# Performance work log

Measured on AMD Instinct MI355X. Metric: run time of the kernel, lower is better.

Reference implementation:

```python
import jax, jax.numpy as jnp
import numpy as np

B, T, N, C = 4, 16, 256, 768
H = 12
D = C // H
HID = 4 * C
SCALE = D ** -0.5
EPS = 1e-5


def _layernorm(x, g, b):
    mu = jnp.mean(x, axis=-1, keepdims=True)
    var = jnp.var(x, axis=-1, keepdims=True)
    return (x - mu) * jax.lax.rsqrt(var + EPS) * g + b


def setup_inputs() -> dict:
    key = jax.random.key(0)
    ks = jax.random.split(key, 12)
    s = 0.02
    return {
        "x": jax.random.normal(ks[0], (B, T, N, C), dtype=jnp.float32),
        "ln1s_g": jnp.ones((C,), jnp.float32), "ln1s_b": jnp.zeros((C,), jnp.float32),
        "ln1t_g": jnp.ones((C,), jnp.float32), "ln1t_b": jnp.zeros((C,), jnp.float32),
        "ln2_g": jnp.ones((C,), jnp.float32), "ln2_b": jnp.zeros((C,), jnp.float32),
        "Wqkv_s": jax.random.normal(ks[1], (C, 3 * C), jnp.float32) * s,
        "Wproj_s": jax.random.normal(ks[2], (C, C), jnp.float32) * s,
        "bproj_s": jnp.zeros((C,), jnp.float32),
        "Wqkv_t": jax.random.normal(ks[3], (C, 3 * C), jnp.float32) * s,
        "Wproj_t": jax.random.normal(ks[4], (C, C), jnp.float32) * s,
        "bproj_t": jnp.zeros((C,), jnp.float32),
        "Wfc1": jax.random.normal(ks[5], (C, HID), jnp.float32) * s,
        "bfc1": jnp.zeros((HID,), jnp.float32),
        "Wfc2": jax.random.normal(ks[6], (HID, C), jnp.float32) * s,
        "bfc2": jnp.zeros((C,), jnp.float32),
    }


def _spatial_attn(x, Wqkv, Wproj, bproj):
    b, t, n, c = x.shape
    qkv = (x @ Wqkv).reshape(b, t, n, 3, H, D)
    q, k, v = jnp.moveaxis(qkv, 3, 0)  # each (B,T,N,H,D)
    attn = jnp.einsum('btnhd,btmhd->bthnm', q, k) * SCALE
    a = jax.nn.softmax(attn, axis=-1)
    o = jnp.einsum('bthnm,btmhd->btnhd', a, v).reshape(b, t, n, c)
    return o @ Wproj + bproj


def _temporal_attn(x, Wqkv, Wproj, bproj):
    b, t, n, c = x.shape
    qkv = (x @ Wqkv).reshape(b, t, n, 3, H, D)
    q, k, v = jnp.moveaxis(qkv, 3, 0)  # each (B,T,N,H,D)
    attn = jnp.einsum('btnhd,bsnhd->bnhts', q, k) * SCALE
    causal = jnp.triu(jnp.ones((t, t), dtype=bool), k=1)  # (T,T) upper mask
    attn = jnp.where(causal, -jnp.inf, attn)
    a = jax.nn.softmax(attn, axis=-1)
    o = jnp.einsum('bnhts,bsnhd->btnhd', a, v).reshape(b, t, n, c)
    return o @ Wproj + bproj


def _mlp(x, W1, b1, W2, b2):
    h = jax.nn.gelu(x @ W1 + b1, approximate=False)
    return h @ W2 + b2


def reference(x, ln1s_g, ln1s_b, ln1t_g, ln1t_b, ln2_g, ln2_b,
              Wqkv_s, Wproj_s, bproj_s, Wqkv_t, Wproj_t, bproj_t,
              Wfc1, bfc1, Wfc2, bfc2):
    x = x + _spatial_attn(_layernorm(x, ln1s_g, ln1s_b), Wqkv_s, Wproj_s, bproj_s)
    x = x + _temporal_attn(_layernorm(x, ln1t_g, ln1t_b), Wqkv_t, Wproj_t, bproj_t)
    x = x + _mlp(_layernorm(x, ln2_g, ln2_b), Wfc1, bfc1, Wfc2, bfc2)
    return x
```

## Files before the change

kernel.cpp:

```cpp
#include <hip/hip_runtime.h>

typedef unsigned short u16;
typedef __attribute__((ext_vector_type(8))) __bf16 bf16x8;
typedef __attribute__((ext_vector_type(4))) float f32x4;
typedef __attribute__((ext_vector_type(4))) u16 u16x4;

#define DEVI static __device__ __forceinline__

DEVI u16 f2bf(float f) {
    unsigned u = __float_as_uint(f);
    u += 0x7fffu + ((u >> 16) & 1u);
    return (u16)(u >> 16);
}
DEVI float bf2f(u16 b) { return __uint_as_float(((unsigned)b) << 16); }

DEVI void gll16(const void* g, void* s) {
    __builtin_amdgcn_global_load_lds((__attribute__((address_space(1))) void*)(g),
                                     (__attribute__((address_space(3))) void*)(s),
                                     16, 0, 0);
}

__global__ __launch_bounds__(256) void wtrans(const float* __restrict__ in,
                                              u16* __restrict__ out, int K, int N) {
    __shared__ float tile[32][33];
    int t = threadIdx.x;
    int n0 = blockIdx.x * 32, k0 = blockIdx.y * 32;
    int r = t >> 3, c4 = (t & 7) << 2;
    float4 v = *(const float4*)(in + (size_t)(k0 + r) * N + n0 + c4);
    tile[r][c4 + 0] = v.x; tile[r][c4 + 1] = v.y;
    tile[r][c4 + 2] = v.z; tile[r][c4 + 3] = v.w;
    __syncthreads();
    u16x4 o;
    o.x = f2bf(tile[c4 + 0][r]);
    o.y = f2bf(tile[c4 + 1][r]);
    o.z = f2bf(tile[c4 + 2][r]);
    o.w = f2bf(tile[c4 + 3][r]);
    *(u16x4*)(out + (size_t)(n0 + r) * K + k0 + c4) = o;
}

__global__ __launch_bounds__(256) void ln_bf16(const float* __restrict__ x,
                                               const float* __restrict__ g,
                                               const float* __restrict__ b,
                                               u16* __restrict__ out) {
    int l = threadIdx.x & 63;
    size_t row = (size_t)blockIdx.x * 4 + (threadIdx.x >> 6);
    const float4* xr = (const float4*)(x + row * 768);
    float4 vv[3];
    vv[0] = xr[l]; vv[1] = xr[l + 64]; vv[2] = xr[l + 128];
    float s = 0.f, ss = 0.f;
#pragma unroll
    for (int i = 0; i < 3; ++i) {
        s  += vv[i].x + vv[i].y + vv[i].z + vv[i].w;
        ss += vv[i].x * vv[i].x + vv[i].y * vv[i].y + vv[i].z * vv[i].z + vv[i].w * vv[i].w;
    }
#pragma unroll
    for (int m = 1; m < 64; m <<= 1) { s += __shfl_xor(s, m); ss += __shfl_xor(ss, m); }
    float mean = s * (1.f / 768.f);
    float rstd = rsqrtf(ss * (1.f / 768.f) - mean * mean + 1e-5f);
    const float4* gr = (const float4*)g;
    const float4* br = (const float4*)b;
    u16* orow = out + row * 768;
#pragma unroll
    for (int i = 0; i < 3; ++i) {
        float4 gv = gr[l + i * 64], bv = br[l + i * 64];
        u16x4 o;
        o.x = f2bf((vv[i].x - mean) * rstd * gv.x + bv.x);
        o.y = f2bf((vv[i].y - mean) * rstd * gv.y + bv.y);
        o.z = f2bf((vv[i].z - mean) * rstd * gv.z + bv.z);
        o.w = f2bf((vv[i].w - mean) * rstd * gv.w + bv.w);
        *(u16x4*)(orow + l * 4 + i * 256) = o;
    }
}

template <int HAS_BIAS, int HAS_RES, int DO_GELU, int OUT_BF16>
__global__ __launch_bounds__(256, 2) void gemm_bf16(const u16* __restrict__ A,
                                                    const u16* __restrict__ BT,
                                                    const float* __restrict__ bias,
                                                    const float* res,
                                                    void* outp, int M, int N, int K) {
    __shared__ __attribute__((aligned(16))) u16 lds_a[128 * 64];
    __shared__ __attribute__((aligned(16))) u16 lds_b[128 * 64];
    const int tid = threadIdx.x, l = tid & 63, w = tid >> 6;
    const int wr = w >> 1, wc = w & 1;
    const int lr = l & 15, lk8 = (l >> 4) * 8;
    const int m0 = blockIdx.y * 128, n0 = blockIdx.x * 128;
    const f32x4 FZ = {0.f, 0.f, 0.f, 0.f};
    f32x4 acc[4][4];
#pragma unroll
    for (int mi = 0; mi < 4; ++mi)
#pragma unroll
        for (int ni = 0; ni < 4; ++ni) acc[mi][ni] = FZ;

    const int nkt = K >> 6;
    for (int kt = 0; kt < nkt; ++kt) {
#pragma unroll
        for (int it = 0; it < 4; ++it) {
            int ci = it * 256 + tid;
            int rowa = ci >> 3, sl = ci & 7;
            gll16(A  + (size_t)(m0 + rowa) * K + kt * 64 + sl * 8, lds_a + ci * 8);
            gll16(BT + (size_t)(n0 + rowa) * K + kt * 64 + sl * 8, lds_b + ci * 8);
        }
        __syncthreads();
#pragma unroll
        for (int ks = 0; ks < 2; ++ks) {
            bf16x8 av[4], bv[4];
#pragma unroll
            for (int mi = 0; mi < 4; ++mi)
                av[mi] = *(const bf16x8*)&lds_a[(wr * 64 + mi * 16 + lr) * 64 + ks * 32 + lk8];
#pragma unroll
            for (int ni = 0; ni < 4; ++ni)
                bv[ni] = *(const bf16x8*)&lds_b[(wc * 64 + ni * 16 + lr) * 64 + ks * 32 + lk8];
#pragma unroll
            for (int mi = 0; mi < 4; ++mi)
#pragma unroll
                for (int ni = 0; ni < 4; ++ni)
                    acc[mi][ni] = __builtin_amdgcn_mfma_f32_16x16x32_bf16(av[mi], bv[ni],
                                                                          acc[mi][ni], 0, 0, 0);
        }
        __syncthreads();
    }
#pragma unroll
    for (int mi = 0; mi < 4; ++mi)
#pragma unroll
        for (int ni = 0; ni < 4; ++ni) {
            int col = n0 + wc * 64 + ni * 16 + lr;
            float bs = HAS_BIAS ? bias[col] : 0.f;
#pragma unroll
            for (int r = 0; r < 4; ++r) {
                int row = m0 + wr * 64 + mi * 16 + (l >> 4) * 4 + r;
                float v = acc[mi][ni][r] + bs;
                if (DO_GELU) v = 0.5f * v * (1.f + erff(v * 0.70710678118654752f));
                size_t idx = (size_t)row * N + col;
                if (HAS_RES) v += res[idx];
                if (OUT_BF16) ((u16*)outp)[idx] = f2bf(v);
                else          ((float*)outp)[idx] = v;
            }
        }
}

__global__ __launch_bounds__(256, 2) void sattn(const u16* __restrict__ qkv,
                                                u16* __restrict__ attno) {
    __shared__ __attribute__((aligned(16))) u16 p_lds[4][16][264];
    __shared__ __attribute__((aligned(16))) u16 vt_lds[64][264];
    const int tid = threadIdx.x, l = tid & 63, w = tid >> 6;
    const int lr = l & 15, lg = l >> 4;
    const int bid = blockIdx.x;
    const int h = bid % 12;
    const size_t R0 = (size_t)(bid / 12) * 256;
    const u16* base = qkv + R0 * 2304;
    const f32x4 FZ = {0.f, 0.f, 0.f, 0.f};

    {
        const u16* vrow = base + (size_t)tid * 2304 + 1536 + h * 64;
#pragma unroll
        for (int c = 0; c < 8; ++c) {
            bf16x8 vv = *(const bf16x8*)(vrow + c * 8);
            const u16* pv = (const u16*)&vv;
#pragma unroll
            for (int e = 0; e < 8; ++e) vt_lds[c * 8 + e][tid] = pv[e];
        }
    }
    __syncthreads();

    u16* attbase = attno + R0 * 768 + h * 64;
    for (int qb = 0; qb < 4; ++qb) {
        const int qrow0 = qb * 64 + w * 16;
        f32x4 acc[16];
#pragma unroll
        for (int nt = 0; nt < 16; ++nt) acc[nt] = FZ;
        const u16* qp = base + (size_t)(qrow0 + lr) * 2304 + h * 64;
#pragma unroll
        for (int ks = 0; ks < 2; ++ks) {
            bf16x8 af = *(const bf16x8*)(qp + ks * 32 + lg * 8);
#pragma unroll
            for (int nt = 0; nt < 16; ++nt) {
                const u16* kp = base + (size_t)(nt * 16 + lr) * 2304 + 768 + h * 64 + ks * 32 + lg * 8;
                bf16x8 bfr = *(const bf16x8*)kp;
                acc[nt] = __builtin_amdgcn_mfma_f32_16x16x32_bf16(af, bfr, acc[nt], 0, 0, 0);
            }
        }
#pragma unroll
        for (int r = 0; r < 4; ++r) {
            float m = acc[0][r] * 0.125f;
#pragma unroll
            for (int nt = 0; nt < 16; ++nt) { acc[nt][r] *= 0.125f; m = fmaxf(m, acc[nt][r]); }
            m = fmaxf(m, __shfl_xor(m, 1));
            m = fmaxf(m, __shfl_xor(m, 2));
            m = fmaxf(m, __shfl_xor(m, 4));
            m = fmaxf(m, __shfl_xor(m, 8));
            float ssum = 0.f;
#pragma unroll
            for (int nt = 0; nt < 16; ++nt) {
                float e = __expf(acc[nt][r] - m);
                acc[nt][r] = e; ssum += e;
            }
            ssum += __shfl_xor(ssum, 1);
            ssum += __shfl_xor(ssum, 2);
            ssum += __shfl_xor(ssum, 4);
            ssum += __shfl_xor(ssum, 8);
            float inv = 1.f / ssum;
#pragma unroll
            for (int nt = 0; nt < 16; ++nt) acc[nt][r] *= inv;
        }
#pragma unroll
        for (int nt = 0; nt < 16; ++nt)
#pragma unroll
            for (int r = 0; r < 4; ++r)
                p_lds[w][lg * 4 + r][nt * 16 + lr] = f2bf(acc[nt][r]);
        __syncthreads();
        f32x4 oacc[4];
#pragma unroll
        for (int dt = 0; dt < 4; ++dt) oacc[dt] = FZ;
#pragma unroll
        for (int ks = 0; ks < 8; ++ks) {
            bf16x8 af = *(const bf16x8*)&p_lds[w][lr][ks * 32 + lg * 8];
#pragma unroll
            for (int dt = 0; dt < 4; ++dt) {
                bf16x8 bfr = *(const bf16x8*)&vt_lds[dt * 16 + lr][ks * 32 + lg * 8];
                oacc[dt] = __builtin_amdgcn_mfma_f32_16x16x32_bf16(af, bfr, oacc[dt], 0, 0, 0);
            }
        }
#pragma unroll
        for (int dt = 0; dt < 4; ++dt)
#pragma unroll
            for (int r = 0; r < 4; ++r)
                attbase[(size_t)(qrow0 + lg * 4 + r) * 768 + dt * 16 + lr] = f2bf(oacc[dt][r]);
        __syncthreads();
    }
}

__global__ __launch_bounds__(256, 4) void tattn(const u16* __restrict__ qkv,
                                                u16* __restrict__ attno) {
    __shared__ float p_lds[4][16][17];
    const int tid = threadIdx.x, l = tid & 63, wv = tid >> 6;
    const int gw = blockIdx.x * 4 + wv;
    const int h = gw % 12;
    const int bn = gw / 12;
    const int n = bn & 255, b = bn >> 8;
    const u16* base = qkv + ((size_t)(b * 16) * 256 + n) * 2304;
    const size_t tstr = (size_t)256 * 2304;
    const int tk = l & 15, g = l >> 4;

    bf16x8 kv[8];
    const u16* kp = base + (size_t)tk * tstr + 768 + h * 64;
#pragma unroll
    for (int c = 0; c < 8; ++c) kv[c] = *(const bf16x8*)(kp + c * 8);

#pragma unroll
    for (int pass = 0; pass < 4; ++pass) {
        int tq = pass * 4 + g;
        const u16* qp = base + (size_t)tq * tstr + h * 64;
        float s = 0.f;
#pragma unroll
        for (int c = 0; c < 8; ++c) {
            bf16x8 qv = *(const bf16x8*)(qp + c * 8);
#pragma unroll
            for (int e = 0; e < 8; ++e) s += (float)qv[e] * (float)kv[c][e];
        }
        s = (tk <= tq) ? s * 0.125f : -1e30f;
        float m = s;
        m = fmaxf(m, __shfl_xor(m, 1));
        m = fmaxf(m, __shfl_xor(m, 2));
        m = fmaxf(m, __shfl_xor(m, 4));
        m = fmaxf(m, __shfl_xor(m, 8));
        float p = __expf(s - m);
        float ssum = p;
        ssum += __shfl_xor(ssum, 1);
        ssum += __shfl_xor(ssum, 2);
        ssum += __shfl_xor(ssum, 4);
        ssum += __shfl_xor(ssum, 8);
        p_lds[wv][tq][tk] = p / ssum;
    }
    __syncthreads();
    float vreg[16];
#pragma unroll
    for (int t2 = 0; t2 < 16; ++t2)
        vreg[t2] = bf2f(base[(size_t)t2 * tstr + 1536 + h * 64 + l]);
    u16* ob = attno + ((size_t)(b * 16) * 256 + n) * 768 + h * 64 + l;
#pragma unroll
    for (int tq = 0; tq < 16; ++tq) {
        float o = 0.f;
#pragma unroll
        for (int t2 = 0; t2 < 16; ++t2) o += p_lds[wv][tq][t2] * vreg[t2];
        ob[(size_t)tq * 256 * 768] = f2bf(o);
    }
}

extern "C" void kernel_launch(void* const* d_in, const int* in_sizes, int n_in,
                              void* d_out, int out_size, void* d_ws, size_t ws_size,
                              hipStream_t stream) {
    (void)in_sizes; (void)n_in; (void)out_size; (void)ws_size;
    const float* x       = (const float*)d_in[0];
    const float* ln1s_g  = (const float*)d_in[1];
    const float* ln1s_b  = (const float*)d_in[2];
    const float* ln1t_g  = (const float*)d_in[3];
    const float* ln1t_b  = (const float*)d_in[4];
    const float* ln2_g   = (const float*)d_in[5];
    const float* ln2_b   = (const float*)d_in[6];
    const float* Wqkv_s  = (const float*)d_in[7];
    const float* Wproj_s = (const float*)d_in[8];
    const float* bproj_s = (const float*)d_in[9];
    const float* Wqkv_t  = (const float*)d_in[10];
    const float* Wproj_t = (const float*)d_in[11];
    const float* bproj_t = (const float*)d_in[12];
    const float* Wfc1    = (const float*)d_in[13];
    const float* bfc1    = (const float*)d_in[14];
    const float* Wfc2    = (const float*)d_in[15];
    const float* bfc2    = (const float*)d_in[16];
    float* out = (float*)d_out;

    const int M = 16384, C = 768, HID = 3072, NQKV = 2304;

    char* p = (char*)d_ws;
    auto carve = [&](size_t bytes) {
        char* r = p;
        p += (bytes + 255) & ~(size_t)255;
        return r;
    };
    u16* wqkvT_s  = (u16*)carve((size_t)NQKV * C * 2);
    u16* wprojT_s = (u16*)carve((size_t)C * C * 2);
    u16* wqkvT_t  = (u16*)carve((size_t)NQKV * C * 2);
    u16* wprojT_t = (u16*)carve((size_t)C * C * 2);
    u16* wfc1T    = (u16*)carve((size_t)HID * C * 2);
    u16* wfc2T    = (u16*)carve((size_t)C * HID * 2);
    u16* xn       = (u16*)carve((size_t)M * C * 2);
    u16* attno    = (u16*)carve((size_t)M * C * 2);
    u16* big      = (u16*)carve((size_t)M * HID * 2);

    wtrans<<<dim3(NQKV / 32, C / 32), 256, 0, stream>>>(Wqkv_s, wqkvT_s, C, NQKV);
    wtrans<<<dim3(C / 32, C / 32), 256, 0, stream>>>(Wproj_s, wprojT_s, C, C);
    wtrans<<<dim3(NQKV / 32, C / 32), 256, 0, stream>>>(Wqkv_t, wqkvT_t, C, NQKV);
    wtrans<<<dim3(C / 32, C / 32), 256, 0, stream>>>(Wproj_t, wprojT_t, C, C);
    wtrans<<<dim3(HID / 32, C / 32), 256, 0, stream>>>(Wfc1, wfc1T, C, HID);
    wtrans<<<dim3(C / 32, HID / 32), 256, 0, stream>>>(Wfc2, wfc2T, HID, C);

    ln_bf16<<<M / 4, 256, 0, stream>>>(x, ln1s_g, ln1s_b, xn);
    gemm_bf16<0, 0, 0, 1><<<dim3(NQKV / 128, M / 128), 256, 0, stream>>>(
        xn, wqkvT_s, nullptr, nullptr, big, M, NQKV, C);
    sattn<<<768, 256, 0, stream>>>(big, attno);
    gemm_bf16<1, 1, 0, 0><<<dim3(C / 128, M / 128), 256, 0, stream>>>(
        attno, wprojT_s, bproj_s, x, out, M, C, C);

    ln_bf16<<<M / 4, 256, 0, stream>>>(out, ln1t_g, ln1t_b, xn);
    gemm_bf16<0, 0, 0, 1><<<dim3(NQKV / 128, M / 128), 256, 0, stream>>>(
        xn, wqkvT_t, nullptr, nullptr, big, M, NQKV, C);
    tattn<<<12288 / 4, 256, 0, stream>>>(big, attno);
    gemm_bf16<1, 1, 0, 0><<<dim3(C / 128, M / 128), 256, 0, stream>>>(
        attno, wprojT_t, bproj_t, out, out, M, C, C);

    ln_bf16<<<M / 4, 256, 0, stream>>>(out, ln2_g, ln2_b, xn);
    gemm_bf16<1, 0, 1, 1><<<dim3(HID / 128, M / 128), 256, 0, stream>>>(
        xn, wfc1T, bfc1, nullptr, big, M, HID, C);
    gemm_bf16<1, 1, 0, 0><<<dim3(C / 128, M / 128), 256, 0, stream>>>(
        big, wfc2T, bfc2, out, out, M, C, HID);
}
```

Before: 648.1 us.

## Replace 128x128 GEMM with pipelined 256x256 double-buffered MFMA kernel

Every dense GEMM now uses a new 512-thread kernel that computes 256x256 output tiles. It double-buffers LDS tiles filled by global_load_lds, issuing loads for later K steps while MFMAs run on the current buffer. The kernel also raises wave priority around MFMA bursts and remaps block IDs across XCDs to improve L2 locality. In exchange, the larger tiles give far fewer blocks for the C=768-wide GEMMs (192 on a 256-CU part), and 128KB of LDS limits occupancy to about one block per CU.

Result: slower. 719.8 us (+11.1%).

```diff
diff --git a/kernel.cpp b/kernel.cpp
--- a/kernel.cpp
+++ b/kernel.cpp
@@ -72,63 +72,130 @@
     }
 }
 
+#define MFMA_(a, b, c) __builtin_amdgcn_mfma_f32_16x16x32_bf16(a, b, c, 0, 0, 0)
+#define BAR() do { __builtin_amdgcn_sched_barrier(0); __builtin_amdgcn_s_barrier(); \
+                   __builtin_amdgcn_sched_barrier(0); } while (0)
+
 template <int HAS_BIAS, int HAS_RES, int DO_GELU, int OUT_BF16>
-__global__ __launch_bounds__(256, 2) void gemm_bf16(const u16* __restrict__ A,
-                                                    const u16* __restrict__ BT,
-                                                    const float* __restrict__ bias,
-                                                    const float* res,
-                                                    void* outp, int M, int N, int K) {
-    __shared__ __attribute__((aligned(16))) u16 lds_a[128 * 64];
-    __shared__ __attribute__((aligned(16))) u16 lds_b[128 * 64];
-    const int tid = threadIdx.x, l = tid & 63, w = tid >> 6;
-    const int wr = w >> 1, wc = w & 1;
-    const int lr = l & 15, lk8 = (l >> 4) * 8;
-    const int m0 = blockIdx.y * 128, n0 = blockIdx.x * 128;
+__global__ __launch_bounds__(512, 2) void gemm256(const u16* __restrict__ A,
+                                                  const u16* __restrict__ BT,
+                                                  const float* __restrict__ bias,
+                                                  const float* res, void* outp,
+                                                  int M, int N, int K, int nbx) {
+    __shared__ __attribute__((aligned(16))) u16 lds_s[2][2][2][8192];
+    const int tid = threadIdx.x, l = tid & 63, wid = tid >> 6;
+    const int l15 = l & 15, lhi = l >> 4;
+    const int wr = wid >> 2, wcn = wid & 3;
+    const int nwg = gridDim.x, orig = blockIdx.x;
+    const int qq = nwg >> 3, xcd = orig & 7, ii = orig >> 3;
+    const int swz = xcd * qq + ii;
+    const int bx = swz % nbx, by = swz / nbx;
+    const int m0 = by * 256, n0 = bx * 256;
+    const int nkt = K >> 6;
+
+    const u16* pA0 = A + (size_t)(m0 + wid * 32 + l15) * K + lhi * 8;
+    const u16* pA1 = pA0 + (size_t)16 * K;
+    const u16* pB0 = BT + (size_t)(n0 + wid * 32 + l15) * K + lhi * 8;
+    const u16* pB1 = pB0 + (size_t)16 * K;
+
+#define STAGE(D, MAT, KS, KT) do {                                          \
+        const int _ko = (KT) * 64 + (KS) * 32;                              \
+        u16* _dst = &lds_s[D][MAT][KS][wid * 1024];                         \
+        gll16(((MAT) ? pB0 : pA0) + _ko, _dst);                             \
+        gll16(((MAT) ? pB1 : pA1) + _ko, _dst + 512);                       \
+    } while (0)
+
+#define LDA_(D, KS, MF) (*(const bf16x8*)&lds_s[D][0][KS][(wr * 8 + (MF)) * 512 + l * 8])
+#define LDB_(D, KS, NF) (*(const bf16x8*)&lds_s[D][1][KS][(wcn * 4 + (NF)) * 512 + l * 8])
+#define LDA4(D, KS, MLO) do { av[0] = LDA_(D, KS, (MLO) + 0); av[1] = LDA_(D, KS, (MLO) + 1); \
+                              av[2] = LDA_(D, KS, (MLO) + 2); av[3] = LDA_(D, KS, (MLO) + 3); } while (0)
+#define LDB4(D, KS) do { bv[0] = LDB_(D, KS, 0); bv[1] = LDB_(D, KS, 1);    \
+                         bv[2] = LDB_(D, KS, 2); bv[3] = LDB_(D, KS, 3); } while (0)
+#define MM16(MLO) do {                                                      \
+        __builtin_amdgcn_s_setprio(1);                                      \
+        acc[(MLO)+0][0] = MFMA_(av[0], bv[0], acc[(MLO)+0][0]);             \
+        acc[(MLO)+0][1] = MFMA_(av[0], bv[1], acc[(MLO)+0][1]);             \
+        acc[(MLO)+0][2] = MFMA_(av[0], bv[2], acc[(MLO)+0][2]);             \
+        acc[(MLO)+0][3] = MFMA_(av[0], bv[3], acc[(MLO)+0][3]);             \
+        acc[(MLO)+1][0] = MFMA_(av[1], bv[0], acc[(MLO)+1][0]);             \
+        acc[(MLO)+1][1] = MFMA_(av[1], bv[1], acc[(MLO)+1][1]);             \
+        acc[(MLO)+1][2] = MFMA_(av[1], bv[2], acc[(MLO)+1][2]);             \
+        acc[(MLO)+1][3] = MFMA_(av[1], bv[3], acc[(MLO)+1][3]);             \
+        acc[(MLO)+2][0] = MFMA_(av[2], bv[0], acc[(MLO)+2][0]);             \
+        acc[(MLO)+2][1] = MFMA_(av[2], bv[1], acc[(MLO)+2][1]);             \
+        acc[(MLO)+2][2] = MFMA_(av[2], bv[2], acc[(MLO)+2][2]);             \
+        acc[(MLO)+2][3] = MFMA_(av[2], bv[3], acc[(MLO)+2][3]);             \
+        acc[(MLO)+3][0] = MFMA_(av[3], bv[0], acc[(MLO)+3][0]);             \
+        acc[(MLO)+3][1] = MFMA_(av[3], bv[1], acc[(MLO)+3][1]);             \
+        acc[(MLO)+3][2] = MFMA_(av[3], bv[2], acc[(MLO)+3][2]);             \
+        acc[(MLO)+3][3] = MFMA_(av[3], bv[3], acc[(MLO)+3][3]);             \
+        __builtin_amdgcn_s_setprio(0);                                      \
+    } while (0)
+
+    f32x4 acc[8][4];
     const f32x4 FZ = {0.f, 0.f, 0.f, 0.f};
-    f32x4 acc[4][4];
-#pragma unroll
-    for (int mi = 0; mi < 4; ++mi)
-#pragma unroll
-        for (int ni = 0; ni < 4; ++ni) acc[mi][ni] = FZ;
-
-    const int nkt = K >> 6;
-    for (int kt = 0; kt < nkt; ++kt) {
-#pragma unroll
-        for (int it = 0; it < 4; ++it) {
-            int ci = it * 256 + tid;
-            int rowa = ci >> 3, sl = ci & 7;
-            gll16(A  + (size_t)(m0 + rowa) * K + kt * 64 + sl * 8, lds_a + ci * 8);
-            gll16(BT + (size_t)(n0 + rowa) * K + kt * 64 + sl * 8, lds_b + ci * 8);
-        }
-        __syncthreads();
-#pragma unroll
-        for (int ks = 0; ks < 2; ++ks) {
-            bf16x8 av[4], bv[4];
-#pragma unroll
-            for (int mi = 0; mi < 4; ++mi)
-                av[mi] = *(const bf16x8*)&lds_a[(wr * 64 + mi * 16 + lr) * 64 + ks * 32 + lk8];
-#pragma unroll
-            for (int ni = 0; ni < 4; ++ni)
-                bv[ni] = *(const bf16x8*)&lds_b[(wc * 64 + ni * 16 + lr) * 64 + ks * 32 + lk8];
-#pragma unroll
-            for (int mi = 0; mi < 4; ++mi)
-#pragma unroll
-                for (int ni = 0; ni < 4; ++ni)
-                    acc[mi][ni] = __builtin_amdgcn_mfma_f32_16x16x32_bf16(av[mi], bv[ni],
-                                                                          acc[mi][ni], 0, 0, 0);
-        }
-        __syncthreads();
-    }
-#pragma unroll
-    for (int mi = 0; mi < 4; ++mi)
-#pragma unroll
-        for (int ni = 0; ni < 4; ++ni) {
-            int col = n0 + wc * 64 + ni * 16 + lr;
-            float bs = HAS_BIAS ? bias[col] : 0.f;
+#pragma unroll
+    for (int mf = 0; mf < 8; ++mf)
+#pragma unroll
+        for (int nf = 0; nf < 4; ++nf) acc[mf][nf] = FZ;
+
+    STAGE(0, 1, 0, 0);
+    STAGE(0, 0, 0, 0);
+    STAGE(0, 1, 1, 0);
+    STAGE(0, 0, 1, 0);
+    STAGE(1, 1, 0, 1);
+    STAGE(1, 0, 0, 1);
+    STAGE(1, 1, 1, 1);
+    asm volatile("s_waitcnt vmcnt(6)" ::: "memory");
+    BAR();
+
+    const int nit = nkt >> 1;
+    for (int it = 0; it < nit; ++it) {
+        const int kt0 = it * 2;
+        const int kt2 = (kt0 + 2 < nkt) ? kt0 + 2 : nkt - 1;
+        const int kt3 = (kt0 + 3 < nkt) ? kt0 + 3 : nkt - 1;
+        bf16x8 av[4], bv[4];
+        LDB4(0, 0); LDA4(0, 0, 0);
+        STAGE(1, 0, 1, kt0 + 1);
+        BAR(); MM16(0); BAR();
+        LDA4(0, 0, 4);
+        STAGE(0, 1, 0, kt2);
+        BAR(); MM16(4); BAR();
+        LDB4(0, 1); LDA4(0, 1, 0);
+        STAGE(0, 0, 0, kt2);
+        BAR(); MM16(0); BAR();
+        LDA4(0, 1, 4);
+        STAGE(0, 1, 1, kt2);
+        BAR(); MM16(4);
+        asm volatile("s_waitcnt vmcnt(6)" ::: "memory");
+        BAR();
+        LDB4(1, 0); LDA4(1, 0, 0);
+        STAGE(0, 0, 1, kt2);
+        BAR(); MM16(0); BAR();
+        LDA4(1, 0, 4);
+        STAGE(1, 1, 0, kt3);
+        BAR(); MM16(4); BAR();
+        LDB4(1, 1); LDA4(1, 1, 0);
+        STAGE(1, 0, 0, kt3);
+        BAR(); MM16(0); BAR();
+        LDA4(1, 1, 4);
+        STAGE(1, 1, 1, kt3);
+        BAR(); MM16(4);
+        asm volatile("s_waitcnt vmcnt(6)" ::: "memory");
+        BAR();
+    }
+    asm volatile("s_waitcnt vmcnt(0)" ::: "memory");
+
+#pragma unroll
+    for (int mf = 0; mf < 8; ++mf)
+#pragma unroll
+        for (int nf = 0; nf < 4; ++nf) {
+            const int col = n0 + wcn * 64 + nf * 16 + l15;
+            const float bs = HAS_BIAS ? bias[col] : 0.f;
 #pragma unroll
             for (int r = 0; r < 4; ++r) {
-                int row = m0 + wr * 64 + mi * 16 + (l >> 4) * 4 + r;
-                float v = acc[mi][ni][r] + bs;
+                const int row = m0 + wr * 128 + mf * 16 + lhi * 4 + r;
+                float v = acc[mf][nf][r] + bs;
                 if (DO_GELU) v = 0.5f * v * (1.f + erff(v * 0.70710678118654752f));
                 size_t idx = (size_t)row * N + col;
                 if (HAS_RES) v += res[idx];
@@ -136,6 +203,12 @@
                 else          ((float*)outp)[idx] = v;
             }
         }
+#undef STAGE
+#undef LDA_
+#undef LDB_
+#undef LDA4
+#undef LDB4
+#undef MM16
 }
 
 __global__ __launch_bounds__(256, 2) void sattn(const u16* __restrict__ qkv,
@@ -335,22 +408,22 @@
     wtrans<<<dim3(C / 32, HID / 32), 256, 0, stream>>>(Wfc2, wfc2T, HID, C);
 
     ln_bf16<<<M / 4, 256, 0, stream>>>(x, ln1s_g, ln1s_b, xn);
-    gemm_bf16<0, 0, 0, 1><<<dim3(NQKV / 128, M / 128), 256, 0, stream>>>(
-        xn, wqkvT_s, nullptr, nullptr, big, M, NQKV, C);
+    gemm256<0, 0, 0, 1><<<(NQKV / 256) * (M / 256), 512, 0, stream>>>(
+        xn, wqkvT_s, nullptr, nullptr, big, M, NQKV, C, NQKV / 256);
     sattn<<<768, 256, 0, stream>>>(big, attno);
-    gemm_bf16<1, 1, 0, 0><<<dim3(C / 128, M / 128), 256, 0, stream>>>(
-        attno, wprojT_s, bproj_s, x, out, M, C, C);
+    gemm256<1, 1, 0, 0><<<(C / 256) * (M / 256), 512, 0, stream>>>(
+        attno, wprojT_s, bproj_s, x, out, M, C, C, C / 256);
 
     ln_bf16<<<M / 4, 256, 0, stream>>>(out, ln1t_g, ln1t_b, xn);
-    gemm_bf16<0, 0, 0, 1><<<dim3(NQKV / 128, M / 128), 256, 0, stream>>>(
-        xn, wqkvT_t, nullptr, nullptr, big, M, NQKV, C);
+    gemm256<0, 0, 0, 1><<<(NQKV / 256) * (M / 256), 512, 0, stream>>>(
+        xn, wqkvT_t, nullptr, nullptr, big, M, NQKV, C, NQKV / 256);
     tattn<<<12288 / 4, 256, 0, stream>>>(big, attno);
-    gemm_bf16<1, 1, 0, 0><<<dim3(C / 128, M / 128), 256, 0, stream>>>(
-        attno, wprojT_t, bproj_t, out, out, M, C, C);
+    gemm256<1, 1, 0, 0><<<(C / 256) * (M / 256), 512, 0, stream>>>(
+        attno, wprojT_t, bproj_t, out, out, M, C, C, C / 256);
 
     ln_bf16<<<M / 4, 256, 0, stream>>>(out, ln2_g, ln2_b, xn);
-    gemm_bf16<1, 0, 1, 1><<<dim3(HID / 128, M / 128), 256, 0, stream>>>(
-        xn, wfc1T, bfc1, nullptr, big, M, HID, C);
-    gemm_bf16<1, 1, 0, 0><<<dim3(C / 128, M / 128), 256, 0, stream>>>(
-        big, wfc2T, bfc2, out, out, M, C, HID);
-}
+    gemm256<1, 0, 1, 1><<<(HID / 256) * (M / 256), 512, 0, stream>>>(
+        xn, wfc1T, bfc1, nullptr, big, M, HID, C, HID / 256);
+    gemm256<1, 1, 0, 0><<<(C / 256) * (M / 256), 512, 0, stream>>>(
+        big, wfc2T, bfc2, out, out, M, C, HID, C / 256);
+}
```

## Rework GEMM with MFMA-fragment LDS layout, staged vectorized epilogue, fast GELU

Applied to the files above, without the earlier changes.

The GEMM's LDS tiles are reorganized so that each global_load_lds writes data directly in the per-lane MFMA fragment order. Fragment reads then become contiguous 16-byte loads, which should avoid bank conflicts from the row-major 64-wide layout. The epilogue stages accumulators through LDS so the output and the residual read can use wide 16-byte vector stores and loads instead of scattered scalar accesses. GELU switches from erff to the Abramowitz-Stegun polynomial with __expf, which is cheaper but carries about 1e-7 approximation error, and occupancy is raised to 4 blocks per SM via launch bounds, which may add register pressure.

New measurement: 796.4 us. 22.9% more time.

```diff
diff --git a/kernel.cpp b/kernel.cpp
--- a/kernel.cpp
+++ b/kernel.cpp
@@ -4,6 +4,7 @@
 typedef __attribute__((ext_vector_type(8))) __bf16 bf16x8;
 typedef __attribute__((ext_vector_type(4))) float f32x4;
 typedef __attribute__((ext_vector_type(4))) u16 u16x4;
+typedef __attribute__((ext_vector_type(8))) u16 u16x8;
 
 #define DEVI static __device__ __forceinline__
 
@@ -13,6 +14,16 @@
     return (u16)(u >> 16);
 }
 DEVI float bf2f(u16 b) { return __uint_as_float(((unsigned)b) << 16); }
+
+DEVI float gelu_f(float v) {
+    float z = fabsf(v) * 0.70710678118654752f;
+    float t = 1.f / (1.f + 0.3275911f * z);
+    float p = t * (0.254829592f + t * (-0.284496736f + t * (1.421413741f +
+              t * (-1.453152027f + t * 1.061405429f))));
+    float erfz = 1.f - p * __expf(-z * z);
+    erfz = (v < 0.f) ? -erfz : erfz;
+    return 0.5f * v * (1.f + erfz);
+}
 
 DEVI void gll16(const void* g, void* s) {
     __builtin_amdgcn_global_load_lds((__attribute__((address_space(1))) void*)(g),
@@ -72,33 +83,44 @@
     }
 }
 
+#define MFMA_(a, b, c) __builtin_amdgcn_mfma_f32_16x16x32_bf16(a, b, c, 0, 0, 0)
+
 template <int HAS_BIAS, int HAS_RES, int DO_GELU, int OUT_BF16>
-__global__ __launch_bounds__(256, 2) void gemm_bf16(const u16* __restrict__ A,
-                                                    const u16* __restrict__ BT,
-                                                    const float* __restrict__ bias,
-                                                    const float* res,
-                                                    void* outp, int M, int N, int K) {
-    __shared__ __attribute__((aligned(16))) u16 lds_a[128 * 64];
-    __shared__ __attribute__((aligned(16))) u16 lds_b[128 * 64];
-    const int tid = threadIdx.x, l = tid & 63, w = tid >> 6;
-    const int wr = w >> 1, wc = w & 1;
-    const int lr = l & 15, lk8 = (l >> 4) * 8;
+__global__ __launch_bounds__(256, 4) void gemm128(const u16* __restrict__ A,
+                                                  const u16* __restrict__ BT,
+                                                  const float* __restrict__ bias,
+                                                  const float* res, void* outp,
+                                                  int M, int N, int K) {
+    __shared__ __attribute__((aligned(16))) u16 lds_s[2][2][4096];
+    const int tid = threadIdx.x, l = tid & 63, wid = tid >> 6;
+    const int l15 = l & 15, lhi = l >> 4;
+    const int wr = wid >> 1, wcn = wid & 1;
     const int m0 = blockIdx.y * 128, n0 = blockIdx.x * 128;
+    const int nkt = K >> 6;
+
+    const u16* pA0 = A + (size_t)(m0 + wid * 32 + l15) * K + lhi * 8;
+    const u16* pA1 = pA0 + (size_t)16 * K;
+    const u16* pB0 = BT + (size_t)(n0 + wid * 32 + l15) * K + lhi * 8;
+    const u16* pB1 = pB0 + (size_t)16 * K;
+
+    f32x4 acc[4][4];
     const f32x4 FZ = {0.f, 0.f, 0.f, 0.f};
-    f32x4 acc[4][4];
-#pragma unroll
-    for (int mi = 0; mi < 4; ++mi)
-#pragma unroll
-        for (int ni = 0; ni < 4; ++ni) acc[mi][ni] = FZ;
-
-    const int nkt = K >> 6;
+#pragma unroll
+    for (int mf = 0; mf < 4; ++mf)
+#pragma unroll
+        for (int nf = 0; nf < 4; ++nf) acc[mf][nf] = FZ;
+
     for (int kt = 0; kt < nkt; ++kt) {
-#pragma unroll
-        for (int it = 0; it < 4; ++it) {
-            int ci = it * 256 + tid;
-            int rowa = ci >> 3, sl = ci & 7;
-            gll16(A  + (size_t)(m0 + rowa) * K + kt * 64 + sl * 8, lds_a + ci * 8);
-            gll16(BT + (size_t)(n0 + rowa) * K + kt * 64 + sl * 8, lds_b + ci * 8);
+        const int ko = kt * 64;
+        {
+            u16* d00 = &lds_s[0][0][wid * 1024];
+            u16* d01 = &lds_s[0][1][wid * 1024];
+            u16* d10 = &lds_s[1][0][wid * 1024];
+            u16* d11 = &lds_s[1][1][wid * 1024];
+            gll16(pA0 + ko,      d00);       gll16(pA1 + ko,      d00 + 512);
+            gll16(pB0 + ko,      d10);       gll16(pB1 + ko,      d10 + 512);
+            gll16(pA0 + ko + 32, d01);       gll16(pA1 + ko + 32, d01 + 512);
+            gll16(pB0 + ko + 32, d11);       gll16(pB1 + ko + 32, d11 + 512);
         }
         __syncthreads();
 #pragma unroll
@@ -106,36 +128,66 @@
             bf16x8 av[4], bv[4];
 #pragma unroll
             for (int mi = 0; mi < 4; ++mi)
-                av[mi] = *(const bf16x8*)&lds_a[(wr * 64 + mi * 16 + lr) * 64 + ks * 32 + lk8];
+                av[mi] = *(const bf16x8*)&lds_s[0][ks][(wr * 4 + mi) * 512 + l * 8];
 #pragma unroll
             for (int ni = 0; ni < 4; ++ni)
-                bv[ni] = *(const bf16x8*)&lds_b[(wc * 64 + ni * 16 + lr) * 64 + ks * 32 + lk8];
+                bv[ni] = *(const bf16x8*)&lds_s[1][ks][(wcn * 4 + ni) * 512 + l * 8];
 #pragma unroll
             for (int mi = 0; mi < 4; ++mi)
 #pragma unroll
                 for (int ni = 0; ni < 4; ++ni)
-                    acc[mi][ni] = __builtin_amdgcn_mfma_f32_16x16x32_bf16(av[mi], bv[ni],
-                                                                          acc[mi][ni], 0, 0, 0);
+                    acc[mi][ni] = MFMA_(av[mi], bv[ni], acc[mi][ni]);
         }
         __syncthreads();
     }
-#pragma unroll
-    for (int mi = 0; mi < 4; ++mi)
-#pragma unroll
-        for (int ni = 0; ni < 4; ++ni) {
-            int col = n0 + wc * 64 + ni * 16 + lr;
-            float bs = HAS_BIAS ? bias[col] : 0.f;
+
+    float* sc = (float*)&lds_s[0][0][0] + (size_t)wid * 1088;
+    float bs[4];
+#pragma unroll
+    for (int nf = 0; nf < 4; ++nf)
+        bs[nf] = HAS_BIAS ? bias[n0 + wcn * 64 + nf * 16 + l15] : 0.f;
+
+#pragma unroll
+    for (int pass = 0; pass < 4; ++pass) {
+        const int mf = pass;
+#pragma unroll
+        for (int nf = 0; nf < 4; ++nf)
 #pragma unroll
             for (int r = 0; r < 4; ++r) {
-                int row = m0 + wr * 64 + mi * 16 + (l >> 4) * 4 + r;
-                float v = acc[mi][ni][r] + bs;
-                if (DO_GELU) v = 0.5f * v * (1.f + erff(v * 0.70710678118654752f));
-                size_t idx = (size_t)row * N + col;
-                if (HAS_RES) v += res[idx];
-                if (OUT_BF16) ((u16*)outp)[idx] = f2bf(v);
-                else          ((float*)outp)[idx] = v;
-            }
-        }
+                float v = acc[mf][nf][r] + bs[nf];
+                if (DO_GELU) v = gelu_f(v);
+                sc[(lhi * 4 + r) * 68 + nf * 16 + l15] = v;
+            }
+        const int rowbase = m0 + wr * 64 + pass * 16;
+        if (OUT_BF16) {
+#pragma unroll
+            for (int itr = 0; itr < 2; ++itr) {
+                const int rr = itr * 8 + (l >> 3);
+                const int c0 = (l & 7) * 8;
+                float4 f0 = *(float4*)&sc[rr * 68 + c0];
+                float4 f1 = *(float4*)&sc[rr * 68 + c0 + 4];
+                u16x8 ov;
+                ov[0] = f2bf(f0.x); ov[1] = f2bf(f0.y);
+                ov[2] = f2bf(f0.z); ov[3] = f2bf(f0.w);
+                ov[4] = f2bf(f1.x); ov[5] = f2bf(f1.y);
+                ov[6] = f2bf(f1.z); ov[7] = f2bf(f1.w);
+                *(u16x8*)((u16*)outp + (size_t)(rowbase + rr) * N + n0 + wcn * 64 + c0) = ov;
+            }
+        } else {
+#pragma unroll
+            for (int itr = 0; itr < 4; ++itr) {
+                const int rr = itr * 4 + lhi;
+                const int c0 = l15 * 4;
+                float4 f0 = *(float4*)&sc[rr * 68 + c0];
+                const size_t idx = (size_t)(rowbase + rr) * N + n0 + wcn * 64 + c0;
+                if (HAS_RES) {
+                    float4 rv = *(const float4*)(res + idx);
+                    f0.x += rv.x; f0.y += rv.y; f0.z += rv.z; f0.w += rv.w;
+                }
+                *(float4*)((float*)outp + idx) = f0;
+            }
+        }
+    }
 }
 
 __global__ __launch_bounds__(256, 2) void sattn(const u16* __restrict__ qkv,
@@ -335,22 +387,22 @@
     wtrans<<<dim3(C / 32, HID / 32), 256, 0, stream>>>(Wfc2, wfc2T, HID, C);
 
     ln_bf16<<<M / 4, 256, 0, stream>>>(x, ln1s_g, ln1s_b, xn);
-    gemm_bf16<0, 0, 0, 1><<<dim3(NQKV / 128, M / 128), 256, 0, stream>>>(
+    gemm128<0, 0, 0, 1><<<dim3(NQKV / 128, M / 128), 256, 0, stream>>>(
         xn, wqkvT_s, nullptr, nullptr, big, M, NQKV, C);
     sattn<<<768, 256, 0, stream>>>(big, attno);
-    gemm_bf16<1, 1, 0, 0><<<dim3(C / 128, M / 128), 256, 0, stream>>>(
+    gemm128<1, 1, 0, 0><<<dim3(C / 128, M / 128), 256, 0, stream>>>(
         attno, wprojT_s, bproj_s, x, out, M, C, C);
 
     ln_bf16<<<M / 4, 256, 0, stream>>>(out, ln1t_g, ln1t_b, xn);
-    gemm_bf16<0, 0, 0, 1><<<dim3(NQKV / 128, M / 128), 256, 0, stream>>>(
+    gemm128<0, 0, 0, 1><<<dim3(NQKV / 128, M / 128), 256, 0, stream>>>(
         xn, wqkvT_t, nullptr, nullptr, big, M, NQKV, C);
     tattn<<<12288 / 4, 256, 0, stream>>>(big, attno);
-    gemm_bf16<1, 1, 0, 0><<<dim3(C / 128, M / 128), 256, 0, stream>>>(
+    gemm128<1, 1, 0, 0><<<dim3(C / 128, M / 128), 256, 0, stream>>>(
         attno, wprojT_t, bproj_t, out, out, M, C, C);
 
     ln_bf16<<<M / 4, 256, 0, stream>>>(out, ln2_g, ln2_b, xn);
-    gemm_bf16<1, 0, 1, 1><<<dim3(HID / 128, M / 128), 256, 0, stream>>>(
+    gemm128<1, 0, 1, 1><<<dim3(HID / 128, M / 128), 256, 0, stream>>>(
         xn, wfc1T, bfc1, nullptr, big, M, HID, C);
-    gemm_bf16<1, 1, 0, 0><<<dim3(C / 128, M / 128), 256, 0, stream>>>(
+    gemm128<1, 1, 0, 0><<<dim3(C / 128, M / 128), 256, 0, stream>>>(
         big, wfc2T, bfc2, out, out, M, C, HID);
 }
```
